# Kernel optimization log

Hardware: AMD Instinct MI355X
Metric: run time of the kernel (lower is better)

The kernel has to match this reference:

```python
import jax, jax.numpy as jnp
import numpy as np


def setup_inputs() -> dict:
    key = jax.random.key(0)
    x = jax.random.normal(key, (4, 256, 64, 64), dtype=jnp.float32)
    return {"x": x}


def reference(x):
    # x: [B, C, W, H]
    B, C, W, H = x.shape
    N = W * H
    q = x.reshape(B, C, N).transpose(0, 2, 1)  # [B, N, C] (proj_query)
    # per-token L2 norm over channels
    q_norm = jnp.linalg.norm(q, ord=2, axis=2)  # [B, N]
    # outer product of norms: [B, N, N]
    nm = q_norm[:, :, None] * q_norm[:, None, :]
    # raw dot-product energy: [B, N, N]
    energy = jnp.einsum('bnc,bmc->bnm', q, q)
    norm_energy = energy / (nm + 1e-6)
    attention = jax.nn.softmax(norm_energy, axis=-1)
    return attention
```

## Files before the change

### kernel.cpp

```cpp
#include <hip/hip_runtime.h>
#include <hip/hip_bf16.h>

#define BATCH 4
#define CDIM  256
#define NTOK  4096

#define BM 64
#define BN 128

typedef short bf16x8 __attribute__((ext_vector_type(8)));
typedef float floatx4 __attribute__((ext_vector_type(4)));
typedef unsigned int uintx4 __attribute__((ext_vector_type(4)));
typedef unsigned int u32;

#define PIN(v) asm volatile("" : "+v"(v))

__device__ inline u32 f2bf1(float f) {
    u32 u = __float_as_uint(f);
    u += 0x7fffu + ((u >> 16) & 1u);
    return u >> 16;
}
__device__ inline u32 f2bf2(float lo, float hi) { return f2bf1(lo) | (f2bf1(hi) << 16); }

__device__ inline void gload_lds16(const short* g, short* l) {
    __builtin_amdgcn_global_load_lds(
        (const __attribute__((address_space(1))) u32*)g,
        (__attribute__((address_space(3))) u32*)l, 16, 0, 0);
}

#define TT 32
__global__ __launch_bounds__(256) void prep_kernel(const float* __restrict__ x,
                                                   short* __restrict__ xn) {
    __shared__ float tile[TT][CDIM + 2];
    __shared__ float part[8][TT];
    __shared__ float rinv_s[TT];
    const int tid = threadIdx.x;
    const int blk = blockIdx.x;
    const int b = blk >> 7;
    const int t0 = (blk & 127) * TT;
    const float* xb = x + (size_t)b * CDIM * NTOK;
    const int ti = tid & 31, cq = tid >> 5;
    float ss = 0.f;
    for (int c = cq; c < CDIM; c += 8) {
        float v = xb[(size_t)c * NTOK + t0 + ti];
        tile[ti][c] = v;
        ss += v * v;
    }
    part[cq][ti] = ss;
    __syncthreads();
    if (tid < TT) {
        float s = 0.f;
#pragma unroll
        for (int q = 0; q < 8; ++q) s += part[q][tid];
        rinv_s[tid] = 1.0f / sqrtf(s);
    }
    __syncthreads();
    const int tok = tid >> 3, seg = tid & 7;
    const float ri = rinv_s[tok];
    size_t obase = ((size_t)(b * NTOK + t0 + tok)) * CDIM + seg * 32;
#pragma unroll
    for (int j = 0; j < 4; ++j) {
        u32 w[4];
#pragma unroll
        for (int u = 0; u < 4; ++u) {
            float f0 = tile[tok][seg * 32 + j * 8 + 2 * u] * ri;
            float f1 = tile[tok][seg * 32 + j * 8 + 2 * u + 1] * ri;
            w[u] = f2bf2(f0, f1);
        }
        *(uintx4*)&xn[obase + j * 8] = (uintx4){w[0], w[1], w[2], w[3]};
    }
}

__global__ __launch_bounds__(512, 2) void attn_kernel(const short* __restrict__ xn,
                                                      float* __restrict__ out) {
    __shared__ short Bs[2][4][128][64];
    __shared__ float rowsumLds[BM][4];
    const int tid = threadIdx.x;
    const int D = blockIdx.x;
    const int b = D >> 6;
    const int rb = (D & 63) * BM;
    const short* xnb = xn + (size_t)b * NTOK * CDIM;
    float* outb = out + ((size_t)b << 24);
    const int lane = tid & 63, wid = tid >> 6;
    const int wr = (wid >> 2) * 32;
    const int wc = (wid & 3) * 32;
    const int r0 = lane & 15, kq = lane >> 4;

    const int trl0 = (wid << 3) + (lane >> 3);
    const int c8 = (lane & 7) ^ (lane >> 3);

    bf16x8 afr[2][8];
#pragma unroll
    for (int m = 0; m < 2; ++m) {
        const short* arow = xnb + (size_t)(rb + wr + m * 16 + r0) * CDIM;
#pragma unroll
        for (int j = 0; j < 8; ++j) {
            afr[m][j] = *(const bf16x8*)(arow + j * 32 + kq * 8);
            PIN(afr[m][j]);
        }
    }

    float psum[2][4] = {{0.f,0.f,0.f,0.f},{0.f,0.f,0.f,0.f}};
    float rinv[2][4];

    auto stage = [&](int ct, int buf) {
        const short* srcBase = xnb + (size_t)(ct * BN) * CDIM;
#pragma unroll
        for (int kc = 0; kc < 4; ++kc)
#pragma unroll
            for (int h = 0; h < 2; ++h) {
                const short* s = srcBase + (size_t)(h * 64 + trl0) * CDIM + kc * 64 + c8 * 8;
                gload_lds16(s, &Bs[buf][kc][h * 64 + (wid << 3)][0]);
            }
    };

    for (int sweep = 0; sweep < 2; ++sweep) {
        stage(0, 0);
        __syncthreads();

        for (int ct = 0; ct < 32; ++ct) {
            const int cur = ct & 1;
            if (ct + 1 < 32) stage(ct + 1, cur ^ 1);

            floatx4 acc[2][2];
#pragma unroll
            for (int m = 0; m < 2; ++m)
#pragma unroll
                for (int n = 0; n < 2; ++n)
                    acc[m][n] = (floatx4){0.f, 0.f, 0.f, 0.f};

            __builtin_amdgcn_s_setprio(1);
#pragma unroll
            for (int kc = 0; kc < 4; ++kc) {
#pragma unroll
                for (int kk = 0; kk < 2; ++kk) {
                    bf16x8 bfr[2];
#pragma unroll
                    for (int n = 0; n < 2; ++n) {
                        const int tr = wc + n * 16 + r0;
                        const int p = ((kk << 2) | kq) ^ (tr & 7);
                        bfr[n] = *(const bf16x8*)&Bs[cur][kc][tr][p * 8];
                    }
                    acc[0][0] = __builtin_amdgcn_mfma_f32_16x16x32_bf16(afr[0][kc*2+kk], bfr[0], acc[0][0], 0,0,0);
                    acc[1][0] = __builtin_amdgcn_mfma_f32_16x16x32_bf16(afr[1][kc*2+kk], bfr[0], acc[1][0], 0,0,0);
                    acc[0][1] = __builtin_amdgcn_mfma_f32_16x16x32_bf16(afr[0][kc*2+kk], bfr[1], acc[0][1], 0,0,0);
                    acc[1][1] = __builtin_amdgcn_mfma_f32_16x16x32_bf16(afr[1][kc*2+kk], bfr[1], acc[1][1], 0,0,0);
                }
            }
            __builtin_amdgcn_s_setprio(0);

            if (sweep == 0) {
#pragma unroll
                for (int m = 0; m < 2; ++m)
#pragma unroll
                    for (int r = 0; r < 4; ++r)
                        psum[m][r] += __expf(acc[m][0][r] - 1.f) + __expf(acc[m][1][r] - 1.f);
            } else {
#pragma unroll
                for (int m = 0; m < 2; ++m)
#pragma unroll
                    for (int r = 0; r < 4; ++r) {
                        const int row = rb + wr + m * 16 + kq * 4 + r;
                        float* p = outb + ((size_t)row << 12) + (ct << 7) + wc + r0;
                        __builtin_nontemporal_store(__expf(acc[m][0][r] - 1.f) * rinv[m][r], p);
                        __builtin_nontemporal_store(__expf(acc[m][1][r] - 1.f) * rinv[m][r], p + 16);
                    }
            }
            __syncthreads();
        }

        if (sweep == 0) {
#pragma unroll
            for (int m = 0; m < 2; ++m)
#pragma unroll
                for (int r = 0; r < 4; ++r) {
                    float v = psum[m][r];
                    v += __shfl_xor(v, 1);
                    v += __shfl_xor(v, 2);
                    v += __shfl_xor(v, 4);
                    v += __shfl_xor(v, 8);
                    if (r0 == 0) rowsumLds[wr + m * 16 + kq * 4 + r][wid & 3] = v;
                }
            __syncthreads();
#pragma unroll
            for (int m = 0; m < 2; ++m)
#pragma unroll
                for (int r = 0; r < 4; ++r) {
                    const int row = wr + m * 16 + kq * 4 + r;
                    rinv[m][r] = 1.0f / (rowsumLds[row][0] + rowsumLds[row][1] +
                                         rowsumLds[row][2] + rowsumLds[row][3]);
                }
            __syncthreads();
        }
    }
}

extern "C" void kernel_launch(void* const* d_in, const int* in_sizes, int n_in,
                              void* d_out, int out_size, void* d_ws, size_t ws_size,
                              hipStream_t stream) {
    const float* x = (const float*)d_in[0];
    float* out = (float*)d_out;
    short* xn = (short*)d_ws;

    prep_kernel<<<BATCH * (NTOK / TT), 256, 0, stream>>>(x, xn);

    attn_kernel<<<NTOK / BM * BATCH, 512, 0, stream>>>(xn, out);
}
```

Before: 160.8 us.

## Replace two-sweep recompute with single GEMM pass, bf16 scratch, and rescale kernel

The fused attention kernel used to run the QK^T GEMM twice: once to get row sums of exp and once to write the normalized output. Now one pass computes exp, stores it as bf16 in a workspace buffer and writes the per-row reciprocal sums. A separate rescale kernel then reads the bf16 scratch and writes the normalized fp32 output. This removes the duplicated GEMM and exp work, but adds 128 MB of scratch writes and reads, uses narrow 2-byte scattered stores, and lowers the precision of the intermediate to bf16.

```diff
diff --git a/kernel.cpp b/kernel.cpp
--- a/kernel.cpp
+++ b/kernel.cpp
@@ -9,6 +9,7 @@
 #define BN 128
 
 typedef short bf16x8 __attribute__((ext_vector_type(8)));
+typedef unsigned short u16x8 __attribute__((ext_vector_type(8)));
 typedef float floatx4 __attribute__((ext_vector_type(4)));
 typedef unsigned int uintx4 __attribute__((ext_vector_type(4)));
 typedef unsigned int u32;
@@ -71,8 +72,9 @@
     }
 }
 
-__global__ __launch_bounds__(512, 2) void attn_kernel(const short* __restrict__ xn,
-                                                      float* __restrict__ out) {
+__global__ __launch_bounds__(512, 2) void exp_kernel(const short* __restrict__ xn,
+                                                     unsigned short* __restrict__ sc,
+                                                     float* __restrict__ rinvG) {
     __shared__ short Bs[2][4][128][64];
     __shared__ float rowsumLds[BM][4];
     const int tid = threadIdx.x;
@@ -80,7 +82,6 @@
     const int b = D >> 6;
     const int rb = (D & 63) * BM;
     const short* xnb = xn + (size_t)b * NTOK * CDIM;
-    float* outb = out + ((size_t)b << 24);
     const int lane = tid & 63, wid = tid >> 6;
     const int wr = (wid >> 2) * 32;
     const int wc = (wid & 3) * 32;
@@ -101,7 +102,6 @@
     }
 
     float psum[2][4] = {{0.f,0.f,0.f,0.f},{0.f,0.f,0.f,0.f}};
-    float rinv[2][4];
 
     auto stage = [&](int ct, int buf) {
         const short* srcBase = xnb + (size_t)(ct * BN) * CDIM;
@@ -114,84 +114,102 @@
             }
     };
 
-    for (int sweep = 0; sweep < 2; ++sweep) {
-        stage(0, 0);
+    stage(0, 0);
+    __syncthreads();
+
+    for (int ct = 0; ct < 32; ++ct) {
+        const int cur = ct & 1;
+        if (ct + 1 < 32) stage(ct + 1, cur ^ 1);
+
+        floatx4 acc[2][2];
+#pragma unroll
+        for (int m = 0; m < 2; ++m)
+#pragma unroll
+            for (int n = 0; n < 2; ++n)
+                acc[m][n] = (floatx4){0.f, 0.f, 0.f, 0.f};
+
+        __builtin_amdgcn_s_setprio(1);
+#pragma unroll
+        for (int kc = 0; kc < 4; ++kc) {
+#pragma unroll
+            for (int kk = 0; kk < 2; ++kk) {
+                bf16x8 bfr[2];
+#pragma unroll
+                for (int n = 0; n < 2; ++n) {
+                    const int tr = wc + n * 16 + r0;
+                    const int p = ((kk << 2) | kq) ^ (tr & 7);
+                    bfr[n] = *(const bf16x8*)&Bs[cur][kc][tr][p * 8];
+                }
+                acc[0][0] = __builtin_amdgcn_mfma_f32_16x16x32_bf16(afr[0][kc*2+kk], bfr[0], acc[0][0], 0,0,0);
+                acc[1][0] = __builtin_amdgcn_mfma_f32_16x16x32_bf16(afr[1][kc*2+kk], bfr[0], acc[1][0], 0,0,0);
+                acc[0][1] = __builtin_amdgcn_mfma_f32_16x16x32_bf16(afr[0][kc*2+kk], bfr[1], acc[0][1], 0,0,0);
+                acc[1][1] = __builtin_amdgcn_mfma_f32_16x16x32_bf16(afr[1][kc*2+kk], bfr[1], acc[1][1], 0,0,0);
+            }
+        }
+        __builtin_amdgcn_s_setprio(0);
+
+        {
+            unsigned short* tileBase = sc + (((size_t)(D * 32 + ct)) << 13);
+#pragma unroll
+            for (int m = 0; m < 2; ++m)
+#pragma unroll
+                for (int r = 0; r < 4; ++r) {
+                    const int rowl = wr + m * 16 + kq * 4 + r;
+#pragma unroll
+                    for (int n = 0; n < 2; ++n) {
+                        float e = __expf(acc[m][n][r] - 1.f);
+                        u32 h = f2bf1(e);
+                        tileBase[rowl * 128 + wc + n * 16 + r0] = (unsigned short)h;
+                        psum[m][r] += __uint_as_float(h << 16);
+                    }
+                }
+        }
         __syncthreads();
-
-        for (int ct = 0; ct < 32; ++ct) {
-            const int cur = ct & 1;
-            if (ct + 1 < 32) stage(ct + 1, cur ^ 1);
-
-            floatx4 acc[2][2];
-#pragma unroll
-            for (int m = 0; m < 2; ++m)
-#pragma unroll
-                for (int n = 0; n < 2; ++n)
-                    acc[m][n] = (floatx4){0.f, 0.f, 0.f, 0.f};
-
-            __builtin_amdgcn_s_setprio(1);
-#pragma unroll
-            for (int kc = 0; kc < 4; ++kc) {
-#pragma unroll
-                for (int kk = 0; kk < 2; ++kk) {
-                    bf16x8 bfr[2];
-#pragma unroll
-                    for (int n = 0; n < 2; ++n) {
-                        const int tr = wc + n * 16 + r0;
-                        const int p = ((kk << 2) | kq) ^ (tr & 7);
-                        bfr[n] = *(const bf16x8*)&Bs[cur][kc][tr][p * 8];
-                    }
-                    acc[0][0] = __builtin_amdgcn_mfma_f32_16x16x32_bf16(afr[0][kc*2+kk], bfr[0], acc[0][0], 0,0,0);
-                    acc[1][0] = __builtin_amdgcn_mfma_f32_16x16x32_bf16(afr[1][kc*2+kk], bfr[0], acc[1][0], 0,0,0);
-                    acc[0][1] = __builtin_amdgcn_mfma_f32_16x16x32_bf16(afr[0][kc*2+kk], bfr[1], acc[0][1], 0,0,0);
-                    acc[1][1] = __builtin_amdgcn_mfma_f32_16x16x32_bf16(afr[1][kc*2+kk], bfr[1], acc[1][1], 0,0,0);
-                }
-            }
-            __builtin_amdgcn_s_setprio(0);
-
-            if (sweep == 0) {
-#pragma unroll
-                for (int m = 0; m < 2; ++m)
-#pragma unroll
-                    for (int r = 0; r < 4; ++r)
-                        psum[m][r] += __expf(acc[m][0][r] - 1.f) + __expf(acc[m][1][r] - 1.f);
-            } else {
-#pragma unroll
-                for (int m = 0; m < 2; ++m)
-#pragma unroll
-                    for (int r = 0; r < 4; ++r) {
-                        const int row = rb + wr + m * 16 + kq * 4 + r;
-                        float* p = outb + ((size_t)row << 12) + (ct << 7) + wc + r0;
-                        __builtin_nontemporal_store(__expf(acc[m][0][r] - 1.f) * rinv[m][r], p);
-                        __builtin_nontemporal_store(__expf(acc[m][1][r] - 1.f) * rinv[m][r], p + 16);
-                    }
-            }
-            __syncthreads();
-        }
-
-        if (sweep == 0) {
-#pragma unroll
-            for (int m = 0; m < 2; ++m)
-#pragma unroll
-                for (int r = 0; r < 4; ++r) {
-                    float v = psum[m][r];
-                    v += __shfl_xor(v, 1);
-                    v += __shfl_xor(v, 2);
-                    v += __shfl_xor(v, 4);
-                    v += __shfl_xor(v, 8);
-                    if (r0 == 0) rowsumLds[wr + m * 16 + kq * 4 + r][wid & 3] = v;
-                }
-            __syncthreads();
-#pragma unroll
-            for (int m = 0; m < 2; ++m)
-#pragma unroll
-                for (int r = 0; r < 4; ++r) {
-                    const int row = wr + m * 16 + kq * 4 + r;
-                    rinv[m][r] = 1.0f / (rowsumLds[row][0] + rowsumLds[row][1] +
-                                         rowsumLds[row][2] + rowsumLds[row][3]);
-                }
-            __syncthreads();
-        }
+    }
+
+#pragma unroll
+    for (int m = 0; m < 2; ++m)
+#pragma unroll
+        for (int r = 0; r < 4; ++r) {
+            float v = psum[m][r];
+            v += __shfl_xor(v, 1);
+            v += __shfl_xor(v, 2);
+            v += __shfl_xor(v, 4);
+            v += __shfl_xor(v, 8);
+            if (r0 == 0) rowsumLds[wr + m * 16 + kq * 4 + r][wid & 3] = v;
+        }
+    __syncthreads();
+    if (tid < BM) {
+        float s = rowsumLds[tid][0] + rowsumLds[tid][1] +
+                  rowsumLds[tid][2] + rowsumLds[tid][3];
+        rinvG[b * NTOK + rb + tid] = 1.0f / s;
+    }
+}
+
+__global__ __launch_bounds__(256) void rescale_kernel(const unsigned short* __restrict__ sc,
+                                                      const float* __restrict__ rinvG,
+                                                      float* __restrict__ out) {
+    const int row = (blockIdx.x << 2) + (threadIdx.x >> 6);
+    const int lane = threadIdx.x & 63;
+    const int rr = row & (NTOK - 1);
+    const int D = ((row >> 12) << 6) + (rr >> 6);
+    const float ri = rinvG[row];
+    float* orow = out + ((size_t)row << 12);
+#pragma unroll
+    for (int it = 0; it < 8; ++it) {
+        const int col = (it << 9) + (lane << 3);
+        const int ct = col >> 7;
+        const unsigned short* p = sc + (((size_t)(D * 32 + ct)) << 13)
+                                + ((rr & 63) << 7) + (col & 127);
+        u16x8 v = *(const u16x8*)p;
+        floatx4 o0, o1;
+#pragma unroll
+        for (int j = 0; j < 4; ++j) {
+            o0[j] = __uint_as_float(((u32)v[j]) << 16) * ri;
+            o1[j] = __uint_as_float(((u32)v[4 + j]) << 16) * ri;
+        }
+        __builtin_nontemporal_store(o0, (floatx4*)&orow[col]);
+        __builtin_nontemporal_store(o1, (floatx4*)&orow[col + 4]);
     }
 }
 
@@ -200,9 +218,12 @@
                               hipStream_t stream) {
     const float* x = (const float*)d_in[0];
     float* out = (float*)d_out;
-    short* xn = (short*)d_ws;
+    char* ws = (char*)d_ws;
+    short* xn = (short*)ws;
+    float* rinvG = (float*)(ws + (8u << 20));
+    unsigned short* sc = (unsigned short*)(ws + (16u << 20));
 
     prep_kernel<<<BATCH * (NTOK / TT), 256, 0, stream>>>(x, xn);
-
-    attn_kernel<<<NTOK / BM * BATCH, 512, 0, stream>>>(xn, out);
-}
+    exp_kernel<<<NTOK / BM * BATCH, 512, 0, stream>>>(xn, sc, rinvG);
+    rescale_kernel<<<(BATCH * NTOK) / 4, 256, 0, stream>>>(sc, rinvG, out);
+}
```

Measured after the change: 197.0 us. +22.5%, slower.

## Pipeline B staging per k-chunk with single LDS buffer and manual vmcnt waits

Applied to the files above, without the earlier changes.

Replaces the double-buffered whole-tile LDS staging with a single buffer split into four k-chunks. Each chunk is refilled two steps ahead, synchronised by explicit s_waitcnt vmcnt counts and raw barriers, and the two sweeps are fully unrolled into macros. This halves LDS usage and overlaps loads with MFMA at a finer grain, aiming to hide global-to-LDS latency and cut barrier stalls. The cost is fragile hand-counted wait values that must account for the outstanding nontemporal stores in sweep two, and more code size.

```diff
diff --git a/kernel.cpp b/kernel.cpp
--- a/kernel.cpp
+++ b/kernel.cpp
@@ -14,6 +14,8 @@
 typedef unsigned int u32;
 
 #define PIN(v) asm volatile("" : "+v"(v))
+#define WAIT(n) asm volatile("s_waitcnt vmcnt(" #n ")" ::: "memory")
+#define BAR() do { __builtin_amdgcn_s_barrier(); asm volatile("" ::: "memory"); } while (0)
 
 __device__ inline u32 f2bf1(float f) {
     u32 u = __float_as_uint(f);
@@ -73,7 +75,7 @@
 
 __global__ __launch_bounds__(512, 2) void attn_kernel(const short* __restrict__ xn,
                                                       float* __restrict__ out) {
-    __shared__ short Bs[2][4][128][64];
+    __shared__ short Bs[4][128][64];
     __shared__ float rowsumLds[BM][4];
     const int tid = threadIdx.x;
     const int D = blockIdx.x;
@@ -85,6 +87,8 @@
     const int wr = (wid >> 2) * 32;
     const int wc = (wid & 3) * 32;
     const int r0 = lane & 15, kq = lane >> 4;
+    const int sx = r0 & 7;
+    const int tr0 = wc + r0, tr1 = wc + 16 + r0;
 
     const int trl0 = (wid << 3) + (lane >> 3);
     const int c8 = (lane & 7) ^ (lane >> 3);
@@ -100,99 +104,125 @@
         }
     }
 
-    float psum[2][4] = {{0.f,0.f,0.f,0.f},{0.f,0.f,0.f,0.f}};
-    float rinv[2][4];
-
-    auto stage = [&](int ct, int buf) {
-        const short* srcBase = xnb + (size_t)(ct * BN) * CDIM;
-#pragma unroll
-        for (int kc = 0; kc < 4; ++kc)
-#pragma unroll
-            for (int h = 0; h < 2; ++h) {
-                const short* s = srcBase + (size_t)(h * 64 + trl0) * CDIM + kc * 64 + c8 * 8;
-                gload_lds16(s, &Bs[buf][kc][h * 64 + (wid << 3)][0]);
-            }
+    float psum0[4] = {0.f, 0.f, 0.f, 0.f}, psum1[4] = {0.f, 0.f, 0.f, 0.f};
+    float rinv0[4], rinv1[4];
+    floatx4 acc00, acc01, acc10, acc11;
+
+    auto stage = [&](int ct, int kc) {
+        const short* s0 = xnb + (size_t)(ct * BN + trl0) * CDIM + kc * 64 + c8 * 8;
+        short* d = &Bs[kc][wid << 3][0];
+        gload_lds16(s0, d);
+        gload_lds16(s0 + (size_t)64 * CDIM, d + 64 * 64);
     };
 
-    for (int sweep = 0; sweep < 2; ++sweep) {
-        stage(0, 0);
-        __syncthreads();
-
-        for (int ct = 0; ct < 32; ++ct) {
-            const int cur = ct & 1;
-            if (ct + 1 < 32) stage(ct + 1, cur ^ 1);
-
-            floatx4 acc[2][2];
-#pragma unroll
-            for (int m = 0; m < 2; ++m)
-#pragma unroll
-                for (int n = 0; n < 2; ++n)
-                    acc[m][n] = (floatx4){0.f, 0.f, 0.f, 0.f};
-
-            __builtin_amdgcn_s_setprio(1);
-#pragma unroll
-            for (int kc = 0; kc < 4; ++kc) {
-#pragma unroll
-                for (int kk = 0; kk < 2; ++kk) {
-                    bf16x8 bfr[2];
-#pragma unroll
-                    for (int n = 0; n < 2; ++n) {
-                        const int tr = wc + n * 16 + r0;
-                        const int p = ((kk << 2) | kq) ^ (tr & 7);
-                        bfr[n] = *(const bf16x8*)&Bs[cur][kc][tr][p * 8];
-                    }
-                    acc[0][0] = __builtin_amdgcn_mfma_f32_16x16x32_bf16(afr[0][kc*2+kk], bfr[0], acc[0][0], 0,0,0);
-                    acc[1][0] = __builtin_amdgcn_mfma_f32_16x16x32_bf16(afr[1][kc*2+kk], bfr[0], acc[1][0], 0,0,0);
-                    acc[0][1] = __builtin_amdgcn_mfma_f32_16x16x32_bf16(afr[0][kc*2+kk], bfr[1], acc[0][1], 0,0,0);
-                    acc[1][1] = __builtin_amdgcn_mfma_f32_16x16x32_bf16(afr[1][kc*2+kk], bfr[1], acc[1][1], 0,0,0);
-                }
-            }
-            __builtin_amdgcn_s_setprio(0);
-
-            if (sweep == 0) {
-#pragma unroll
-                for (int m = 0; m < 2; ++m)
-#pragma unroll
-                    for (int r = 0; r < 4; ++r)
-                        psum[m][r] += __expf(acc[m][0][r] - 1.f) + __expf(acc[m][1][r] - 1.f);
-            } else {
-#pragma unroll
-                for (int m = 0; m < 2; ++m)
-#pragma unroll
-                    for (int r = 0; r < 4; ++r) {
-                        const int row = rb + wr + m * 16 + kq * 4 + r;
-                        float* p = outb + ((size_t)row << 12) + (ct << 7) + wc + r0;
-                        __builtin_nontemporal_store(__expf(acc[m][0][r] - 1.f) * rinv[m][r], p);
-                        __builtin_nontemporal_store(__expf(acc[m][1][r] - 1.f) * rinv[m][r], p + 16);
-                    }
-            }
-            __syncthreads();
+#define ACCZERO() do { acc00 = (floatx4){0,0,0,0}; acc01 = (floatx4){0,0,0,0}; \
+                       acc10 = (floatx4){0,0,0,0}; acc11 = (floatx4){0,0,0,0}; } while (0)
+
+#define COMPUTE(KC) do { \
+    __builtin_amdgcn_s_setprio(1); \
+    const int p0 = kq ^ sx, p1 = (4 | kq) ^ sx; \
+    bf16x8 b0a = *(const bf16x8*)&Bs[KC][tr0][p0 * 8]; \
+    bf16x8 b1a = *(const bf16x8*)&Bs[KC][tr1][p0 * 8]; \
+    bf16x8 b0b = *(const bf16x8*)&Bs[KC][tr0][p1 * 8]; \
+    bf16x8 b1b = *(const bf16x8*)&Bs[KC][tr1][p1 * 8]; \
+    acc00 = __builtin_amdgcn_mfma_f32_16x16x32_bf16(afr[0][(KC)*2],   b0a, acc00, 0,0,0); \
+    acc10 = __builtin_amdgcn_mfma_f32_16x16x32_bf16(afr[1][(KC)*2],   b0a, acc10, 0,0,0); \
+    acc01 = __builtin_amdgcn_mfma_f32_16x16x32_bf16(afr[0][(KC)*2],   b1a, acc01, 0,0,0); \
+    acc11 = __builtin_amdgcn_mfma_f32_16x16x32_bf16(afr[1][(KC)*2],   b1a, acc11, 0,0,0); \
+    acc00 = __builtin_amdgcn_mfma_f32_16x16x32_bf16(afr[0][(KC)*2+1], b0b, acc00, 0,0,0); \
+    acc10 = __builtin_amdgcn_mfma_f32_16x16x32_bf16(afr[1][(KC)*2+1], b0b, acc10, 0,0,0); \
+    acc01 = __builtin_amdgcn_mfma_f32_16x16x32_bf16(afr[0][(KC)*2+1], b1b, acc01, 0,0,0); \
+    acc11 = __builtin_amdgcn_mfma_f32_16x16x32_bf16(afr[1][(KC)*2+1], b1b, acc11, 0,0,0); \
+    __builtin_amdgcn_s_setprio(0); \
+} while (0)
+
+#define STEP(KC, SCT, SKC, WN) do { stage((SCT), (SKC)); WAIT(WN); BAR(); COMPUTE(KC); } while (0)
+#define STEPNS(KC, WN)        do { WAIT(WN); BAR(); COMPUTE(KC); } while (0)
+
+#define EPI0() do { \
+    _Pragma("unroll") for (int r = 0; r < 4; ++r) { \
+        psum0[r] += __expf(acc00[r] - 1.f) + __expf(acc01[r] - 1.f); \
+        psum1[r] += __expf(acc10[r] - 1.f) + __expf(acc11[r] - 1.f); } \
+} while (0)
+
+#define EPI1(CT) do { \
+    _Pragma("unroll") for (int r = 0; r < 4; ++r) { \
+        const int row_a = rb + wr + kq * 4 + r; \
+        float* pa = outb + ((size_t)row_a << 12) + ((CT) << 7) + wc + r0; \
+        __builtin_nontemporal_store(__expf(acc00[r] - 1.f) * rinv0[r], pa); \
+        __builtin_nontemporal_store(__expf(acc01[r] - 1.f) * rinv0[r], pa + 16); \
+        float* pb = pa + ((size_t)16 << 12); \
+        __builtin_nontemporal_store(__expf(acc10[r] - 1.f) * rinv1[r], pb); \
+        __builtin_nontemporal_store(__expf(acc11[r] - 1.f) * rinv1[r], pb + 16); } \
+} while (0)
+
+    stage(0, 0); stage(0, 1);
+    for (int ct = 0; ct < 31; ++ct) {
+        ACCZERO();
+        STEP(0, ct, 2, 4);
+        STEP(1, ct, 3, 4);
+        STEP(2, ct + 1, 0, 4);
+        STEP(3, ct + 1, 1, 4);
+        EPI0();
+    }
+    ACCZERO();
+    STEP(0, 31, 2, 4);
+    STEP(1, 31, 3, 4);
+    STEPNS(2, 2);
+    STEPNS(3, 0);
+    EPI0();
+
+#pragma unroll
+    for (int r = 0; r < 4; ++r) {
+        float v0 = psum0[r], v1 = psum1[r];
+        v0 += __shfl_xor(v0, 1); v0 += __shfl_xor(v0, 2);
+        v0 += __shfl_xor(v0, 4); v0 += __shfl_xor(v0, 8);
+        v1 += __shfl_xor(v1, 1); v1 += __shfl_xor(v1, 2);
+        v1 += __shfl_xor(v1, 4); v1 += __shfl_xor(v1, 8);
+        if (r0 == 0) {
+            rowsumLds[wr + kq * 4 + r][wid & 3] = v0;
+            rowsumLds[wr + 16 + kq * 4 + r][wid & 3] = v1;
         }
-
-        if (sweep == 0) {
-#pragma unroll
-            for (int m = 0; m < 2; ++m)
-#pragma unroll
-                for (int r = 0; r < 4; ++r) {
-                    float v = psum[m][r];
-                    v += __shfl_xor(v, 1);
-                    v += __shfl_xor(v, 2);
-                    v += __shfl_xor(v, 4);
-                    v += __shfl_xor(v, 8);
-                    if (r0 == 0) rowsumLds[wr + m * 16 + kq * 4 + r][wid & 3] = v;
-                }
-            __syncthreads();
-#pragma unroll
-            for (int m = 0; m < 2; ++m)
-#pragma unroll
-                for (int r = 0; r < 4; ++r) {
-                    const int row = wr + m * 16 + kq * 4 + r;
-                    rinv[m][r] = 1.0f / (rowsumLds[row][0] + rowsumLds[row][1] +
-                                         rowsumLds[row][2] + rowsumLds[row][3]);
-                }
-            __syncthreads();
-        }
-    }
+    }
+    __syncthreads();
+#pragma unroll
+    for (int r = 0; r < 4; ++r) {
+        const int ra = wr + kq * 4 + r, rbw = wr + 16 + kq * 4 + r;
+        rinv0[r] = 1.0f / (rowsumLds[ra][0] + rowsumLds[ra][1] + rowsumLds[ra][2] + rowsumLds[ra][3]);
+        rinv1[r] = 1.0f / (rowsumLds[rbw][0] + rowsumLds[rbw][1] + rowsumLds[rbw][2] + rowsumLds[rbw][3]);
+    }
+    __syncthreads();
+
+    stage(0, 0); stage(0, 1);
+    {
+        ACCZERO();
+        STEP(0, 0, 2, 4);
+        STEP(1, 0, 3, 4);
+        STEP(2, 1, 0, 4);
+        STEP(3, 1, 1, 4);
+        EPI1(0);
+    }
+    for (int ct = 1; ct < 31; ++ct) {
+        ACCZERO();
+        STEP(0, ct, 2, 12);
+        STEP(1, ct, 3, 12);
+        STEP(2, ct + 1, 0, 4);
+        STEP(3, ct + 1, 1, 4);
+        EPI1(ct);
+    }
+    ACCZERO();
+    STEP(0, 31, 2, 12);
+    STEP(1, 31, 3, 12);
+    STEPNS(2, 2);
+    STEPNS(3, 0);
+    EPI1(31);
+
+#undef ACCZERO
+#undef COMPUTE
+#undef STEP
+#undef STEPNS
+#undef EPI0
+#undef EPI1
 }
 
 extern "C" void kernel_launch(void* const* d_in, const int* in_sizes, int n_in,
@@ -203,6 +233,5 @@
     short* xn = (short*)d_ws;
 
     prep_kernel<<<BATCH * (NTOK / TT), 256, 0, stream>>>(x, xn);
-
     attn_kernel<<<NTOK / BM * BATCH, 512, 0, stream>>>(xn, out);
 }
```

Measured after the change: 143.8 us. -10.6%, faster.
